# Kernel optimization log

Measured on AMD Instinct MI355X. Metric: run time of the kernel, lower is better.

The kernel has to match this reference:

```python
import jax, jax.numpy as jnp
import numpy as np

FEAT_SIZE, HIDDEN_SIZE, ATT_SIZE = 2048, 1024, 512
BATCH, FEAT_NUM = 64, 512


def setup_inputs() -> dict:
    key = jax.random.key(0)
    ks = jax.random.split(key, 8)
    s = lambda fan_in: 1.0 / np.sqrt(fan_in)
    return {
        "feats": jax.random.normal(ks[0], (BATCH, FEAT_NUM, FEAT_SIZE), jnp.float32),
        "key": jax.random.normal(ks[1], (BATCH, HIDDEN_SIZE), jnp.float32),
        "wh_w": jax.random.uniform(ks[2], (ATT_SIZE, HIDDEN_SIZE), jnp.float32, -s(HIDDEN_SIZE), s(HIDDEN_SIZE)),
        "wh_b": jax.random.uniform(ks[3], (ATT_SIZE,), jnp.float32, -s(HIDDEN_SIZE), s(HIDDEN_SIZE)),
        "wv_w": jax.random.uniform(ks[4], (ATT_SIZE, FEAT_SIZE), jnp.float32, -s(FEAT_SIZE), s(FEAT_SIZE)),
        "wv_b": jax.random.uniform(ks[5], (ATT_SIZE,), jnp.float32, -s(FEAT_SIZE), s(FEAT_SIZE)),
        "wa_w": jax.random.uniform(ks[6], (1, ATT_SIZE), jnp.float32, -s(ATT_SIZE), s(ATT_SIZE)),
    }


def reference(feats, key, wh_w, wh_b, wv_w, wv_b, wa_w):
    # v = wv(feats): (B, N, A)
    v = jnp.einsum('bnf,af->bna', feats, wv_w) + wv_b
    # h = wh(key): (B, A), broadcast-added over feat_num
    h = key @ wh_w.T + wh_b
    inputs = h[:, None, :] + v                       # (B, N, A)
    scores = jnp.einsum('bna,a->bn', jnp.tanh(inputs), wa_w[0])  # (B, N)
    alpha = jax.nn.softmax(scores, axis=1)           # (B, N)
    att_feats = jnp.einsum('bn,bnf->bf', alpha, feats)  # (B, F)
    return (att_feats, alpha)
```

## Files before the change

### kernel.cpp

```cpp
#include <hip/hip_runtime.h>
#include <hip/hip_bf16.h>

#define FEATSZ 2048
#define HIDSZ  1024
#define ATTSZ  512
#define BATCH  64
#define FEATN  512

typedef float  f32x4  __attribute__((ext_vector_type(4)));
typedef __bf16 bf16x8 __attribute__((ext_vector_type(8)));

__device__ __forceinline__ unsigned short f2bf(float f) {
    union { float f; unsigned int u; } x; x.f = f;
    unsigned int u = x.u;
    return (unsigned short)((u + 0x7fffu + ((u >> 16) & 1u)) >> 16);
}

__global__ void k_h(const float* __restrict__ key, const float* __restrict__ wh_w,
                    const float* __restrict__ wh_b, float* __restrict__ h) {
    const int b = blockIdx.y;
    const int ac = blockIdx.x;
    const int t = threadIdx.x;
    const int lane = t & 63, wv = t >> 6;
    float k16[16];
    const float* kb = key + b * HIDSZ;
#pragma unroll
    for (int j = 0; j < 16; ++j) k16[j] = kb[lane + 64 * j];
#pragma unroll 1
    for (int i = 0; i < 16; ++i) {
        int a = ac * 64 + wv * 16 + i;
        const float* wr = wh_w + (size_t)a * HIDSZ;
        float s = 0.f;
#pragma unroll
        for (int j = 0; j < 16; ++j) s += k16[j] * wr[lane + 64 * j];
#pragma unroll
        for (int d = 32; d; d >>= 1) s += __shfl_xor(s, d);
        if (lane == 0) h[b * ATTSZ + a] = s + wh_b[a];
    }
}

__global__ void k_wvcvt(const float* __restrict__ wv_w, unsigned short* __restrict__ wvb) {
    int idx = blockIdx.x * 256 + threadIdx.x;
    int a = idx >> 11, k = idx & 2047;
    int CF = a >> 4, c = a & 15, ks = k >> 5, kin = k & 31;
    int lane = c + ((kin >> 3) << 4);
    int dst = ((ks * 32 + CF) * 64 + lane) * 8 + (kin & 7);
    wvb[dst] = f2bf(wv_w[idx]);
}

__global__ __launch_bounds__(512, 2) void k_scores(
        const float* __restrict__ feats, const unsigned short* __restrict__ wvb,
        const float* __restrict__ h, const float* __restrict__ wv_b,
        const float* __restrict__ wa, float* __restrict__ scores) {
    __shared__ __align__(16) char smem[65536];
    const int t = threadIdx.x;
    const int lane = t & 63, w = t >> 6;
    const int m0 = blockIdx.x * 128;
    const int b = blockIdx.x >> 2;

    const char* fbase = (const char*)feats;
    unsigned int goff[4], ldst[4];
#pragma unroll
    for (int s = 0; s < 4; ++s) {
        int q = w * 256 + s * 64 + lane;
        int r = q >> 4, c = (q & 15) ^ (r & 7);
        goff[s] = (unsigned int)(((m0 + r) * 2048 + c * 4) * 4);
        ldst[s] = (unsigned int)(w * 4096 + s * 1024);
    }
    auto stage = [&](int buf, int it) {
#pragma unroll
        for (int s = 0; s < 4; ++s)
            __builtin_amdgcn_global_load_lds(
                (const __attribute__((address_space(1))) void*)(fbase + goff[s] + it * 256),
                (__attribute__((address_space(3))) void*)(smem + buf * 32768 + ldst[s]),
                16, 0, 0);
    };

    const unsigned short* wb = wvb + lane * 8;
    bf16x8 bnA[4], bnB[4];
    auto loadBA = [&](int kk) {
#pragma unroll
        for (int cf = 0; cf < 4; ++cf) bnA[cf] = *(const bf16x8*)(wb + (kk * 32 + w * 4 + cf) * 512);
    };
    auto loadBB = [&](int kk) {
#pragma unroll
        for (int cf = 0; cf < 4; ++cf) bnB[cf] = *(const bf16x8*)(wb + (kk * 32 + w * 4 + cf) * 512);
    };

    const int sw = lane & 7, kq2 = (lane >> 4) * 2;
    const int off0 = (lane & 15) * 256 + ((kq2    ) ^ sw) * 16;
    const int off1 = (lane & 15) * 256 + ((kq2 | 1) ^ sw) * 16;

    f32x4 acc[8][4];
#pragma unroll
    for (int m = 0; m < 8; ++m)
#pragma unroll
        for (int cf = 0; cf < 4; ++cf) acc[m][cf] = (f32x4)0.0f;

    stage(0, 0);
    loadBA(0);
    __syncthreads();

    auto domfmaA = [&](int buf, int ks) {
#pragma unroll
        for (int m = 0; m < 8; ++m) {
            const char* ap = smem + buf * 32768 + m * 4096 + ks * 128;
            f32x4 fa = *(const f32x4*)__builtin_assume_aligned(ap + off0, 16);
            f32x4 fb = *(const f32x4*)__builtin_assume_aligned(ap + off1, 16);
            bf16x8 af;
            af[0] = (__bf16)fa[0]; af[1] = (__bf16)fa[1]; af[2] = (__bf16)fa[2]; af[3] = (__bf16)fa[3];
            af[4] = (__bf16)fb[0]; af[5] = (__bf16)fb[1]; af[6] = (__bf16)fb[2]; af[7] = (__bf16)fb[3];
#pragma unroll
            for (int cf = 0; cf < 4; ++cf)
                acc[m][cf] = __builtin_amdgcn_mfma_f32_16x16x32_bf16(af, bnA[cf], acc[m][cf], 0, 0, 0);
        }
    };
    auto domfmaB = [&](int buf, int ks) {
#pragma unroll
        for (int m = 0; m < 8; ++m) {
            const char* ap = smem + buf * 32768 + m * 4096 + ks * 128;
            f32x4 fa = *(const f32x4*)__builtin_assume_aligned(ap + off0, 16);
            f32x4 fb = *(const f32x4*)__builtin_assume_aligned(ap + off1, 16);
            bf16x8 af;
            af[0] = (__bf16)fa[0]; af[1] = (__bf16)fa[1]; af[2] = (__bf16)fa[2]; af[3] = (__bf16)fa[3];
            af[4] = (__bf16)fb[0]; af[5] = (__bf16)fb[1]; af[6] = (__bf16)fb[2]; af[7] = (__bf16)fb[3];
#pragma unroll
            for (int cf = 0; cf < 4; ++cf)
                acc[m][cf] = __builtin_amdgcn_mfma_f32_16x16x32_bf16(af, bnB[cf], acc[m][cf], 0, 0, 0);
        }
    };

#pragma unroll 1
    for (int it = 0; it < 32; ++it) {
        const int buf = it & 1;
        if (it < 31) stage(buf ^ 1, it + 1);
        loadBB(2 * it + 1);
        domfmaA(buf, 0);
        loadBA(2 * it + 2 > 63 ? 63 : 2 * it + 2);
        domfmaB(buf, 1);
        __syncthreads();
    }

    const int c16 = lane & 15, q4 = lane >> 4;
    float hreg[4], wreg[4];
#pragma unroll
    for (int cf = 0; cf < 4; ++cf) {
        int a = w * 64 + cf * 16 + c16;
        hreg[cf] = h[b * ATTSZ + a] + wv_b[a];
        wreg[cf] = wa[a];
    }
    float p[8][4];
#pragma unroll
    for (int m = 0; m < 8; ++m)
#pragma unroll
        for (int j = 0; j < 4; ++j) p[m][j] = 0.f;
#pragma unroll
    for (int m = 0; m < 8; ++m)
#pragma unroll
        for (int cf = 0; cf < 4; ++cf)
#pragma unroll
            for (int j = 0; j < 4; ++j)
                p[m][j] += tanhf(acc[m][cf][j] + hreg[cf]) * wreg[cf];
#pragma unroll
    for (int m = 0; m < 8; ++m)
#pragma unroll
        for (int j = 0; j < 4; ++j) {
            float v = p[m][j];
            v += __shfl_xor(v, 1); v += __shfl_xor(v, 2);
            v += __shfl_xor(v, 4); v += __shfl_xor(v, 8);
            p[m][j] = v;
        }
    float* scp = (float*)smem;
    if (c16 == 0) {
#pragma unroll
        for (int m = 0; m < 8; ++m)
#pragma unroll
            for (int j = 0; j < 4; ++j)
                scp[w * 128 + m * 16 + q4 * 4 + j] = p[m][j];
    }
    __syncthreads();
    if (t < 128) {
        float s = 0.f;
#pragma unroll
        for (int ww = 0; ww < 8; ++ww) s += scp[ww * 128 + t];
        scores[m0 + t] = s;
    }
}

__global__ void k_softmax(const float* __restrict__ scores, float* __restrict__ alpha) {
    __shared__ float red[16];
    const int b = blockIdx.x, t = threadIdx.x;
    const int lane = t & 63, w = t >> 6;
    float s = scores[b * FEATN + t];
    float m = s;
#pragma unroll
    for (int d = 32; d; d >>= 1) m = fmaxf(m, __shfl_xor(m, d));
    if (lane == 0) red[w] = m;
    __syncthreads();
    if (t == 0) {
        float mm = red[0];
        for (int i = 1; i < 8; ++i) mm = fmaxf(mm, red[i]);
        red[8] = mm;
    }
    __syncthreads();
    float e = __expf(s - red[8]);
    float sum = e;
#pragma unroll
    for (int d = 32; d; d >>= 1) sum += __shfl_xor(sum, d);
    if (lane == 0) red[w] = sum;
    __syncthreads();
    if (t == 0) {
        float ss = 0.f;
        for (int i = 0; i < 8; ++i) ss += red[i];
        red[9] = 1.0f / ss;
    }
    __syncthreads();
    alpha[b * FEATN + t] = e * red[9];
}

__global__ void k_att_part(const float* __restrict__ feats, const float* __restrict__ alpha,
                           float* __restrict__ part) {
    const int b = blockIdx.x, fc = blockIdx.y, ns = blockIdx.z, t = threadIdx.x;
    const int f0 = fc * 1024 + t * 4;
    const float* fp = feats + (size_t)(b * FEATN + ns * 128) * FEATSZ + f0;
    const float* al = alpha + b * FEATN + ns * 128;
    float4 acc = {0.f, 0.f, 0.f, 0.f};
#pragma unroll 4
    for (int i = 0; i < 128; ++i) {
        float a = al[i];
        float4 v = *(const float4*)(fp + (size_t)i * FEATSZ);
        acc.x += a * v.x; acc.y += a * v.y; acc.z += a * v.z; acc.w += a * v.w;
    }
    *(float4*)(part + ((size_t)ns * BATCH + b) * FEATSZ + f0) = acc;
}

__global__ void k_att_red(const float* __restrict__ part, float* __restrict__ out) {
    const int idx = (blockIdx.x * 256 + threadIdx.x) * 4;
    float4 s = *(const float4*)(part + idx);
#pragma unroll
    for (int z = 1; z < 4; ++z) {
        float4 v = *(const float4*)(part + (size_t)z * (BATCH * FEATSZ) + idx);
        s.x += v.x; s.y += v.y; s.z += v.z; s.w += v.w;
    }
    *(float4*)(out + idx) = s;
}

extern "C" void kernel_launch(void* const* d_in, const int* in_sizes, int n_in,
                              void* d_out, int out_size, void* d_ws, size_t ws_size,
                              hipStream_t stream) {
    const float* feats = (const float*)d_in[0];
    const float* key   = (const float*)d_in[1];
    const float* wh_w  = (const float*)d_in[2];
    const float* wh_b  = (const float*)d_in[3];
    const float* wv_w  = (const float*)d_in[4];
    const float* wv_b  = (const float*)d_in[5];
    const float* wa_w  = (const float*)d_in[6];

    float* out_att   = (float*)d_out;
    float* out_alpha = out_att + BATCH * FEATSZ;

    char* ws = (char*)d_ws;
    float* h              = (float*)(ws);
    float* scores         = (float*)(ws + 131072);
    unsigned short* wvb   = (unsigned short*)(ws + 262144);
    float* part           = (float*)(ws + 262144);

    hipLaunchKernelGGL(k_h,        dim3(8, 64),    dim3(256), 0, stream, key, wh_w, wh_b, h);
    hipLaunchKernelGGL(k_wvcvt,    dim3(4096),     dim3(256), 0, stream, wv_w, wvb);
    hipLaunchKernelGGL(k_scores,   dim3(256),      dim3(512), 0, stream, feats, wvb, h, wv_b, wa_w, scores);
    hipLaunchKernelGGL(k_softmax,  dim3(64),       dim3(512), 0, stream, scores, out_alpha);
    hipLaunchKernelGGL(k_att_part, dim3(64, 2, 4), dim3(256), 0, stream, feats, out_alpha, part);
    hipLaunchKernelGGL(k_att_red,  dim3(128),      dim3(256), 0, stream, part, out_att);
}
```

Measured before the change: 164.1 us.

## Use four-stage LDS ring with finer k-steps and manual vmcnt waits in scores GEMM

The scores GEMM now stages feats in four 16KB LDS buffers of 32 k-elements each instead of two 32KB buffers of 64, prefetching two stages ahead. Each iteration waits with an explicit partial vmcnt and a raw s_barrier in place of a full __syncthreads, with sched_barriers pinning the order of loads and MFMAs. The aim is to keep global-to-LDS loads in flight across barriers and hide memory latency better. The cost is more barriers per k, and correctness now depends on the hand-counted vmcnt values.

Measured after the change: 165.4 us. Within noise of the previous version (+0.8%).

```diff
diff --git a/kernel.cpp b/kernel.cpp
--- a/kernel.cpp
+++ b/kernel.cpp
@@ -52,44 +52,46 @@
         const float* __restrict__ feats, const unsigned short* __restrict__ wvb,
         const float* __restrict__ h, const float* __restrict__ wv_b,
         const float* __restrict__ wa, float* __restrict__ scores) {
-    __shared__ __align__(16) char smem[65536];
+    __shared__ __align__(16) char smem[4][16384];
     const int t = threadIdx.x;
     const int lane = t & 63, w = t >> 6;
     const int m0 = blockIdx.x * 128;
     const int b = blockIdx.x >> 2;
 
     const char* fbase = (const char*)feats;
-    unsigned int goff[4], ldst[4];
-#pragma unroll
-    for (int s = 0; s < 4; ++s) {
-        int q = w * 256 + s * 64 + lane;
-        int r = q >> 4, c = (q & 15) ^ (r & 7);
+    unsigned int goff[2], ldst[2];
+#pragma unroll
+    for (int s = 0; s < 2; ++s) {
+        int q = w * 128 + s * 64 + lane;
+        int r = q >> 3, c = (q & 7) ^ ((q >> 3) & 7);
         goff[s] = (unsigned int)(((m0 + r) * 2048 + c * 4) * 4);
-        ldst[s] = (unsigned int)(w * 4096 + s * 1024);
-    }
-    auto stage = [&](int buf, int it) {
-#pragma unroll
-        for (int s = 0; s < 4; ++s)
+        ldst[s] = (unsigned int)((w * 128 + s * 64) * 16);
+    }
+    auto stage = [&](int buf, int j) {
+#pragma unroll
+        for (int s = 0; s < 2; ++s)
             __builtin_amdgcn_global_load_lds(
-                (const __attribute__((address_space(1))) void*)(fbase + goff[s] + it * 256),
-                (__attribute__((address_space(3))) void*)(smem + buf * 32768 + ldst[s]),
+                (const __attribute__((address_space(1))) void*)(fbase + goff[s] + j * 128),
+                (__attribute__((address_space(3))) void*)(&smem[buf][0] + ldst[s]),
                 16, 0, 0);
     };
 
     const unsigned short* wb = wvb + lane * 8;
-    bf16x8 bnA[4], bnB[4];
+    bf16x8 BA[4], BB[4];
     auto loadBA = [&](int kk) {
 #pragma unroll
-        for (int cf = 0; cf < 4; ++cf) bnA[cf] = *(const bf16x8*)(wb + (kk * 32 + w * 4 + cf) * 512);
+        for (int cf = 0; cf < 4; ++cf)
+            BA[cf] = *(const bf16x8*)(wb + (size_t)(kk * 32 + w * 4 + cf) * 512);
     };
     auto loadBB = [&](int kk) {
 #pragma unroll
-        for (int cf = 0; cf < 4; ++cf) bnB[cf] = *(const bf16x8*)(wb + (kk * 32 + w * 4 + cf) * 512);
+        for (int cf = 0; cf < 4; ++cf)
+            BB[cf] = *(const bf16x8*)(wb + (size_t)(kk * 32 + w * 4 + cf) * 512);
     };
 
     const int sw = lane & 7, kq2 = (lane >> 4) * 2;
-    const int off0 = (lane & 15) * 256 + ((kq2    ) ^ sw) * 16;
-    const int off1 = (lane & 15) * 256 + ((kq2 | 1) ^ sw) * 16;
+    const int off0 = (lane & 15) * 128 + ((kq2    ) ^ sw) * 16;
+    const int off1 = (lane & 15) * 128 + ((kq2 | 1) ^ sw) * 16;
 
     f32x4 acc[8][4];
 #pragma unroll
@@ -97,48 +99,40 @@
 #pragma unroll
         for (int cf = 0; cf < 4; ++cf) acc[m][cf] = (f32x4)0.0f;
 
-    stage(0, 0);
-    loadBA(0);
-    __syncthreads();
-
-    auto domfmaA = [&](int buf, int ks) {
+    auto domfma = [&](const char* ab, bf16x8 (&B)[4]) {
 #pragma unroll
         for (int m = 0; m < 8; ++m) {
-            const char* ap = smem + buf * 32768 + m * 4096 + ks * 128;
-            f32x4 fa = *(const f32x4*)__builtin_assume_aligned(ap + off0, 16);
-            f32x4 fb = *(const f32x4*)__builtin_assume_aligned(ap + off1, 16);
+            f32x4 fa = *(const f32x4*)__builtin_assume_aligned(ab + m * 2048 + off0, 16);
+            f32x4 fb = *(const f32x4*)__builtin_assume_aligned(ab + m * 2048 + off1, 16);
             bf16x8 af;
             af[0] = (__bf16)fa[0]; af[1] = (__bf16)fa[1]; af[2] = (__bf16)fa[2]; af[3] = (__bf16)fa[3];
             af[4] = (__bf16)fb[0]; af[5] = (__bf16)fb[1]; af[6] = (__bf16)fb[2]; af[7] = (__bf16)fb[3];
 #pragma unroll
             for (int cf = 0; cf < 4; ++cf)
-                acc[m][cf] = __builtin_amdgcn_mfma_f32_16x16x32_bf16(af, bnA[cf], acc[m][cf], 0, 0, 0);
+                acc[m][cf] = __builtin_amdgcn_mfma_f32_16x16x32_bf16(af, B[cf], acc[m][cf], 0, 0, 0);
         }
     };
-    auto domfmaB = [&](int buf, int ks) {
-#pragma unroll
-        for (int m = 0; m < 8; ++m) {
-            const char* ap = smem + buf * 32768 + m * 4096 + ks * 128;
-            f32x4 fa = *(const f32x4*)__builtin_assume_aligned(ap + off0, 16);
-            f32x4 fb = *(const f32x4*)__builtin_assume_aligned(ap + off1, 16);
-            bf16x8 af;
-            af[0] = (__bf16)fa[0]; af[1] = (__bf16)fa[1]; af[2] = (__bf16)fa[2]; af[3] = (__bf16)fa[3];
-            af[4] = (__bf16)fb[0]; af[5] = (__bf16)fb[1]; af[6] = (__bf16)fb[2]; af[7] = (__bf16)fb[3];
-#pragma unroll
-            for (int cf = 0; cf < 4; ++cf)
-                acc[m][cf] = __builtin_amdgcn_mfma_f32_16x16x32_bf16(af, bnB[cf], acc[m][cf], 0, 0, 0);
-        }
-    };
-
-#pragma unroll 1
-    for (int it = 0; it < 32; ++it) {
-        const int buf = it & 1;
-        if (it < 31) stage(buf ^ 1, it + 1);
-        loadBB(2 * it + 1);
-        domfmaA(buf, 0);
-        loadBA(2 * it + 2 > 63 ? 63 : 2 * it + 2);
-        domfmaB(buf, 1);
-        __syncthreads();
+
+    stage(0, 0);
+    stage(1, 1);
+    loadBA(0);
+    asm volatile("s_waitcnt vmcnt(6)" ::: "memory");
+    __builtin_amdgcn_s_barrier();
+    __builtin_amdgcn_sched_barrier(0);
+
+#pragma unroll 4
+    for (int j = 0; j < 64; ++j) {
+        const int buf = j & 3;
+        if ((j & 1) == 0) { if (j < 63) loadBB(j + 1); }
+        else             { if (j < 63) loadBA(j + 1); }
+        if (j < 62) stage((j + 2) & 3, j + 2);
+        __builtin_amdgcn_sched_barrier(0);
+        if ((j & 1) == 0) domfma(&smem[buf][0], BA);
+        else              domfma(&smem[buf][0], BB);
+        __builtin_amdgcn_sched_barrier(0);
+        asm volatile("s_waitcnt vmcnt(4)" ::: "memory");
+        __builtin_amdgcn_s_barrier();
+        __builtin_amdgcn_sched_barrier(0);
     }
 
     const int c16 = lane & 15, q4 = lane >> 4;
@@ -149,34 +143,35 @@
         hreg[cf] = h[b * ATTSZ + a] + wv_b[a];
         wreg[cf] = wa[a];
     }
-    float p[8][4];
-#pragma unroll
-    for (int m = 0; m < 8; ++m)
-#pragma unroll
-        for (int j = 0; j < 4; ++j) p[m][j] = 0.f;
+    float pv[8][4];
+#pragma unroll
+    for (int m = 0; m < 8; ++m)
+#pragma unroll
+        for (int j = 0; j < 4; ++j) pv[m][j] = 0.f;
 #pragma unroll
     for (int m = 0; m < 8; ++m)
 #pragma unroll
         for (int cf = 0; cf < 4; ++cf)
 #pragma unroll
             for (int j = 0; j < 4; ++j)
-                p[m][j] += tanhf(acc[m][cf][j] + hreg[cf]) * wreg[cf];
+                pv[m][j] += tanhf(acc[m][cf][j] + hreg[cf]) * wreg[cf];
 #pragma unroll
     for (int m = 0; m < 8; ++m)
 #pragma unroll
         for (int j = 0; j < 4; ++j) {
-            float v = p[m][j];
+            float v = pv[m][j];
             v += __shfl_xor(v, 1); v += __shfl_xor(v, 2);
             v += __shfl_xor(v, 4); v += __shfl_xor(v, 8);
-            p[m][j] = v;
+            pv[m][j] = v;
         }
     float* scp = (float*)smem;
+    __syncthreads();
     if (c16 == 0) {
 #pragma unroll
         for (int m = 0; m < 8; ++m)
 #pragma unroll
             for (int j = 0; j < 4; ++j)
-                scp[w * 128 + m * 16 + q4 * 4 + j] = p[m][j];
+                scp[w * 128 + m * 16 + q4 * 4 + j] = pv[m][j];
     }
     __syncthreads();
     if (t < 128) {
@@ -260,10 +255,10 @@
     float* out_alpha = out_att + BATCH * FEATSZ;
 
     char* ws = (char*)d_ws;
-    float* h              = (float*)(ws);
-    float* scores         = (float*)(ws + 131072);
-    unsigned short* wvb   = (unsigned short*)(ws + 262144);
-    float* part           = (float*)(ws + 262144);
+    float* h            = (float*)(ws);
+    float* scores       = (float*)(ws + 131072);
+    unsigned short* wvb = (unsigned short*)(ws + 262144);
+    float* part         = (float*)(ws + 262144);
 
     hipLaunchKernelGGL(k_h,        dim3(8, 64),    dim3(256), 0, stream, key, wh_w, wh_b, h);
     hipLaunchKernelGGL(k_wvcvt,    dim3(4096),     dim3(256), 0, stream, wv_w, wvb);
```
